# Kernel tuning notes

Measured on AMD Instinct MI355X. Metric: run time of the kernel, lower is better.

The kernel has to match this reference:

```python
import jax, jax.numpy as jnp
import numpy as np

N_NODES = 100000
N_EDGES = 1600000
IN_C, HID_C, OUT_C = 64, 64, 40


def setup_inputs() -> dict:
    key = jax.random.key(0)
    ks = jax.random.split(key, 8)
    x = jax.random.normal(ks[0], (N_NODES, IN_C), dtype=jnp.float32)
    edge_index = jax.random.randint(ks[1], (2, N_EDGES), 0, N_NODES, dtype=jnp.int32)
    s = 1.0 / np.sqrt(HID_C)
    W1 = jax.random.uniform(ks[2], (IN_C, HID_C), jnp.float32, -s, s)
    b1 = jnp.zeros((HID_C,), jnp.float32)
    Wh = jax.random.uniform(ks[3], (HID_C, HID_C), jnp.float32, -s, s)
    bh = jnp.zeros((HID_C,), jnp.float32)
    W2 = jax.random.uniform(ks[4], (HID_C, OUT_C), jnp.float32, -s, s)
    b2 = jnp.zeros((OUT_C,), jnp.float32)
    return {"x": x, "edge_index": edge_index, "W1": W1, "b1": b1,
            "Wh": Wh, "bh": bh, "W2": W2, "b2": b2}


def reference(x, edge_index, W1, b1, Wh, bh, W2, b2):
    N = x.shape[0]
    loop = jnp.arange(N, dtype=edge_index.dtype)
    # GCN normalization with self-loops: A_hat = D^-1/2 (A + I) D^-1/2
    src = jnp.concatenate([edge_index[0], loop])  # [E + N]
    dst = jnp.concatenate([edge_index[1], loop])
    deg = jax.ops.segment_sum(jnp.ones_like(dst, dtype=x.dtype), dst, num_segments=N)
    dinv = jnp.where(deg > 0, jax.lax.rsqrt(deg), 0.0)
    norm = dinv[src] * dinv[dst]  # [E + N]

    def gcn_conv(h, W, b):
        h = h @ W                              # [N, out]
        msg = h[src] * norm[:, None]           # gather + scale, [E+N, out]
        return jax.ops.segment_sum(msg, dst, num_segments=N) + b

    h = jax.nn.relu(gcn_conv(x, W1, b1))       # conv1 (dropout = identity in eval)
    h = jax.nn.relu(gcn_conv(h, Wh, bh))       # hidden_conv, layer_size=2 -> one pass
    h = gcn_conv(h, W2, b2)                    # conv2
    return jax.nn.log_softmax(h, axis=1)
```

## Files before the change

kernel.cpp:

```cpp
#include <hip/hip_runtime.h>
#include <hip/hip_bf16.h>
#include <math.h>

#define EPT 16
#define BUK 256
#define BCAP 4608
#define NBUKMAX 512
#define CAP 64

typedef _Float16 half8 __attribute__((ext_vector_type(8)));
typedef _Float16 half2v __attribute__((ext_vector_type(2)));
typedef float f32x4 __attribute__((ext_vector_type(4)));

__device__ __forceinline__ unsigned short f16r(float f) {
    _Float16 h = (_Float16)f;
    return __builtin_bit_cast(unsigned short, h);
}
__device__ __forceinline__ half2v h2(unsigned u) {
    return __builtin_bit_cast(half2v, u);
}


__launch_bounds__(256, 8)
__global__ void scat1_kernel(const int* __restrict__ src, const int* __restrict__ dst,
                             int* __restrict__ cntg, unsigned* __restrict__ ebuf,
                             int E, int nbuk) {
    __shared__ int lh[NBUKMAX];
    __shared__ int lbase[NBUKMAX];
    int tid = threadIdx.x;
    for (int k = tid; k < nbuk; k += 256) lh[k] = 0;
    __syncthreads();
    int base = blockIdx.x * (256 * EPT);
    int ds[EPT], ss[EPT];
#pragma unroll
    for (int k = 0; k < EPT; ++k) {
        int e = base + k * 256 + tid;
        ds[k] = (e < E) ? dst[e] : -1;
        ss[k] = (e < E) ? src[e] : 0;
    }
#pragma unroll
    for (int k = 0; k < EPT; ++k) {
        if (ds[k] >= 0) atomicAdd(&lh[ds[k] >> 8], 1);
    }
    __syncthreads();
    for (int k = tid; k < nbuk; k += 256) {
        int c = lh[k];
        if (c > 0) lbase[k] = atomicAdd(&cntg[k], c);
        lh[k] = 0;
    }
    __syncthreads();
#pragma unroll
    for (int k = 0; k < EPT; ++k) {
        if (ds[k] >= 0) {
            int b = ds[k] >> 8;
            int pos = lbase[b] + atomicAdd(&lh[b], 1);
            if (pos < BCAP)
                ebuf[(size_t)b * BCAP + pos] = ((unsigned)ss[k] << 8) | (unsigned)(ds[k] & 255);
        }
    }
}


__global__ void build_kernel(const unsigned* __restrict__ ebuf, const int* __restrict__ cntg,
                             int* __restrict__ deg, int* __restrict__ col, int N) {
    __shared__ int hist[BUK];
    __shared__ int cur[BUK];
    int b = blockIdx.x;
    int tid = threadIdx.x;
    int cnt = cntg[b];
    if (cnt > BCAP) cnt = BCAP;
    hist[tid] = 0;
    __syncthreads();
    size_t rbase = (size_t)b * BCAP;
    for (int j = tid; j < cnt; j += 256) {
        atomicAdd(&hist[ebuf[rbase + j] & 255u], 1);
    }
    __syncthreads();
    int node = (b << 8) + tid;
    int d = hist[tid];
    if (d > CAP) d = CAP;
    if (node < N) deg[node] = d;
    cur[tid] = node << 6;
    __syncthreads();
    for (int j = tid; j < cnt; j += 256) {
        unsigned rec = ebuf[rbase + j];
        int ln = rec & 255u;
        int pos = atomicAdd(&cur[ln], 1);
        if (pos < ((((b << 8) + ln) << 6) + CAP)) col[pos] = (int)(rec >> 8);
    }
}


__global__ void prep_kernel(const int* __restrict__ deg, float* __restrict__ dinv,
                            const float* __restrict__ x, unsigned short* __restrict__ xb,
                            const float* __restrict__ W1, const float* __restrict__ Wh,
                            const float* __restrict__ W2, unsigned short* __restrict__ wp1,
                            unsigned short* __restrict__ wph, unsigned short* __restrict__ wp2,
                            int N, int zrow) {
    int bid = blockIdx.x;
    int tid = threadIdx.x;
    if (bid < 16) {
        int i = bid * 256 + tid;
        int j = i & 7;
        int lane = (i >> 3) & 63;
        int hh = (i >> 9) & 1;
        int t = i >> 10;
        int k = hh * 32 + (lane >> 4) * 8 + j;
        int cc = t * 16 + (lane & 15);
        wp1[i] = f16r(W1[k * 64 + cc]);
        wph[i] = f16r(Wh[k * 64 + cc]);
        if (t < 3) wp2[i] = f16r(cc < 40 ? W2[k * 40 + cc] : 0.f);
        if (bid == 0 && tid < 8) {
            *(uint4*)(xb + (size_t)zrow * 64 + tid * 8) = make_uint4(0, 0, 0, 0);
        }
        return;
    }
    int i = (bid - 16) * 256 + tid;
    if (i < N * 16) {
        int node = i >> 4;
        float dn = rsqrtf((float)deg[node] + 1.0f);
        if ((i & 15) == 0) dinv[node] = dn;
        float4 vv = ((const float4*)x)[(size_t)node * 16 + (i & 15)];
        ushort4 o;
        o.x = f16r(vv.x * dn); o.y = f16r(vv.y * dn);
        o.z = f16r(vv.z * dn); o.w = f16r(vv.w * dn);
        ((ushort4*)xb)[(size_t)node * 16 + (i & 15)] = o;
    }
}


__launch_bounds__(256, 8)
__global__ void fused_relu_kernel(const unsigned short* __restrict__ h,
                                  const int* __restrict__ degA,
                                  const int* __restrict__ col,
                                  const float* __restrict__ dinv,
                                  const unsigned short* __restrict__ wp,
                                  const float* __restrict__ bias,
                                  unsigned short* __restrict__ out,
                                  int n, int zrow) {
    __shared__ unsigned short tile[16][72];
    if (blockIdx.x == 0 && threadIdx.x < 8) {
        *(uint4*)(out + (size_t)zrow * 64 + threadIdx.x * 8) = make_uint4(0, 0, 0, 0);
    }
    int tid = threadIdx.x;
    int w = tid >> 6;
    int lane = tid & 63;
    int g = lane >> 4;
    int li = lane & 15;
    int sub = li >> 3;
    unsigned choff = (li & 7) * 16u;
    int nodeBase = blockIdx.x * 16;
    int row = w * 4 + g;
    int node = nodeBase + row;

    int beg = node << 6;
    int deg = -1;
    float di = 0.f;
    if (node < n) {
        deg = degA[node];
        di = dinv[node];
    }
    int total = deg + 1;
    int nb = (total + 15) >> 4;
    nb = max(nb, __shfl_xor(nb, 16));
    nb = max(nb, __shfl_xor(nb, 32));

    half2v a0 = (half2v)0, a1 = (half2v)0, a2 = (half2v)0, a3 = (half2v)0;
    half2v c0 = (half2v)0, c1 = (half2v)0, c2 = (half2v)0, c3 = (half2v)0;

    int idx;
    {
        int e0 = li;
        idx = zrow;
        if (e0 < deg) idx = col[beg + e0];
        else if (e0 == deg) idx = node;
    }
    for (int b = 0; b < nb; ++b) {
        int nidx = zrow;
        if (b + 1 < nb) {
            int e0 = ((b + 1) << 4) + li;
            if (e0 < deg) nidx = col[beg + e0];
            else if (e0 == deg) nidx = node;
        }
        uint4 u[8];
#pragma unroll
        for (int it = 0; it < 8; ++it) {
            int s = __shfl(idx, (g << 4) + it * 2 + sub);
            u[it] = *(const uint4*)((const char*)h + (((unsigned)s << 7) + choff));
        }
        __builtin_amdgcn_sched_barrier(0);
#pragma unroll
        for (int it = 0; it < 8; ++it) {
            if (it & 1) { c0 += h2(u[it].x); c1 += h2(u[it].y); c2 += h2(u[it].z); c3 += h2(u[it].w); }
            else        { a0 += h2(u[it].x); a1 += h2(u[it].y); a2 += h2(u[it].z); a3 += h2(u[it].w); }
        }
        idx = nidx;
    }
    a0 += c0; a1 += c1; a2 += c2; a3 += c3;
    a0 += __builtin_bit_cast(half2v, __shfl_xor(__builtin_bit_cast(int, a0), 8));
    a1 += __builtin_bit_cast(half2v, __shfl_xor(__builtin_bit_cast(int, a1), 8));
    a2 += __builtin_bit_cast(half2v, __shfl_xor(__builtin_bit_cast(int, a2), 8));
    a3 += __builtin_bit_cast(half2v, __shfl_xor(__builtin_bit_cast(int, a3), 8));

    if (sub == 0) {
        half2v dih = __builtin_bit_cast(half2v, __builtin_amdgcn_cvt_pkrtz(di, di));
        a0 *= dih; a1 *= dih; a2 *= dih; a3 *= dih;
        uint4 o;
        o.x = __builtin_bit_cast(unsigned, a0);
        o.y = __builtin_bit_cast(unsigned, a1);
        o.z = __builtin_bit_cast(unsigned, a2);
        o.w = __builtin_bit_cast(unsigned, a3);
        *(uint4*)((char*)&tile[row][0] + choff) = o;
    }
    __syncthreads();

    int q = lane >> 4, c = lane & 15;
    half8 bf0 = *(const half8*)(wp + w * 1024 + lane * 8);
    half8 bf1 = *(const half8*)(wp + w * 1024 + 512 + lane * 8);
    float bs = bias[w * 16 + c];
    half8 fa0 = *(const half8*)&tile[c][q * 8];
    half8 fa1 = *(const half8*)&tile[c][32 + q * 8];
    f32x4 z = {0.f, 0.f, 0.f, 0.f};
    z = __builtin_amdgcn_mfma_f32_16x16x32_f16(fa0, bf0, z, 0, 0, 0);
    z = __builtin_amdgcn_mfma_f32_16x16x32_f16(fa1, bf1, z, 0, 0, 0);
#pragma unroll
    for (int r = 0; r < 4; ++r) {
        int nodeW = nodeBase + q * 4 + r;
        if (nodeW < n) {
            float dn = dinv[nodeW];
            out[(size_t)nodeW * 64 + w * 16 + c] = f16r(fmaxf(z[r] + bs, 0.f) * dn);
        }
    }
}


__launch_bounds__(256, 8)
__global__ void fused_lsm_kernel(const unsigned short* __restrict__ h,
                                 const int* __restrict__ degA,
                                 const int* __restrict__ col,
                                 const float* __restrict__ dinv,
                                 const unsigned short* __restrict__ wp,
                                 const float* __restrict__ bias,
                                 float* __restrict__ out,
                                 int n, int zrow) {
    __shared__ unsigned short tile[16][72];
    int tid = threadIdx.x;
    int w = tid >> 6;
    int lane = tid & 63;
    int g = lane >> 4;
    int li = lane & 15;
    int sub = li >> 3;
    unsigned choff = (li & 7) * 16u;
    int nodeBase = blockIdx.x * 16;
    int row = w * 4 + g;
    int node = nodeBase + row;

    int beg = node << 6;
    int deg = -1;
    float di = 0.f;
    if (node < n) {
        deg = degA[node];
        di = dinv[node];
    }
    int total = deg + 1;
    int nb = (total + 15) >> 4;
    nb = max(nb, __shfl_xor(nb, 16));
    nb = max(nb, __shfl_xor(nb, 32));

    half2v a0 = (half2v)0, a1 = (half2v)0, a2 = (half2v)0, a3 = (half2v)0;
    half2v c0a = (half2v)0, c1a = (half2v)0, c2a = (half2v)0, c3a = (half2v)0;

    int idx;
    {
        int e0 = li;
        idx = zrow;
        if (e0 < deg) idx = col[beg + e0];
        else if (e0 == deg) idx = node;
    }
    for (int b = 0; b < nb; ++b) {
        int nidx = zrow;
        if (b + 1 < nb) {
            int e0 = ((b + 1) << 4) + li;
            if (e0 < deg) nidx = col[beg + e0];
            else if (e0 == deg) nidx = node;
        }
        uint4 u[8];
#pragma unroll
        for (int it = 0; it < 8; ++it) {
            int s = __shfl(idx, (g << 4) + it * 2 + sub);
            u[it] = *(const uint4*)((const char*)h + (((unsigned)s << 7) + choff));
        }
        __builtin_amdgcn_sched_barrier(0);
#pragma unroll
        for (int it = 0; it < 8; ++it) {
            if (it & 1) { c0a += h2(u[it].x); c1a += h2(u[it].y); c2a += h2(u[it].z); c3a += h2(u[it].w); }
            else        { a0 += h2(u[it].x);  a1 += h2(u[it].y);  a2 += h2(u[it].z);  a3 += h2(u[it].w); }
        }
        idx = nidx;
    }
    a0 += c0a; a1 += c1a; a2 += c2a; a3 += c3a;
    a0 += __builtin_bit_cast(half2v, __shfl_xor(__builtin_bit_cast(int, a0), 8));
    a1 += __builtin_bit_cast(half2v, __shfl_xor(__builtin_bit_cast(int, a1), 8));
    a2 += __builtin_bit_cast(half2v, __shfl_xor(__builtin_bit_cast(int, a2), 8));
    a3 += __builtin_bit_cast(half2v, __shfl_xor(__builtin_bit_cast(int, a3), 8));

    if (sub == 0) {
        half2v dih = __builtin_bit_cast(half2v, __builtin_amdgcn_cvt_pkrtz(di, di));
        a0 *= dih; a1 *= dih; a2 *= dih; a3 *= dih;
        uint4 o;
        o.x = __builtin_bit_cast(unsigned, a0);
        o.y = __builtin_bit_cast(unsigned, a1);
        o.z = __builtin_bit_cast(unsigned, a2);
        o.w = __builtin_bit_cast(unsigned, a3);
        *(uint4*)((char*)&tile[row][0] + choff) = o;
    }
    __syncthreads();
    if (w != 0) return;

    int q = lane >> 4, c = lane & 15;
    bool v2ok = (c < 8);

    half8 bfrag[3][2];
#pragma unroll
    for (int t = 0; t < 3; ++t)
#pragma unroll
        for (int hh = 0; hh < 2; ++hh)
            bfrag[t][hh] = *(const half8*)(wp + t * 1024 + hh * 512 + lane * 8);
    float bs[3];
    bs[0] = bias[c];
    bs[1] = bias[16 + c];
    bs[2] = v2ok ? bias[32 + c] : 0.f;

    half8 fa0 = *(const half8*)&tile[c][q * 8];
    half8 fa1 = *(const half8*)&tile[c][32 + q * 8];

    f32x4 acc[3];
#pragma unroll
    for (int t = 0; t < 3; ++t) {
        f32x4 z = {0.f, 0.f, 0.f, 0.f};
        z = __builtin_amdgcn_mfma_f32_16x16x32_f16(fa0, bfrag[t][0], z, 0, 0, 0);
        z = __builtin_amdgcn_mfma_f32_16x16x32_f16(fa1, bfrag[t][1], z, 0, 0, 0);
        acc[t] = z;
    }

#pragma unroll
    for (int r = 0; r < 4; ++r) {
        int nodeW = nodeBase + q * 4 + r;
        if (nodeW < n) {
            float v0 = acc[0][r] + bs[0];
            float v1 = acc[1][r] + bs[1];
            float v2 = v2ok ? (acc[2][r] + bs[2]) : -INFINITY;
            float m = fmaxf(fmaxf(v0, v1), v2);
#pragma unroll
            for (int off = 1; off <= 8; off <<= 1) m = fmaxf(m, __shfl_xor(m, off));
            float s = expf(v0 - m) + expf(v1 - m) + (v2ok ? expf(v2 - m) : 0.f);
#pragma unroll
            for (int off = 1; off <= 8; off <<= 1) s += __shfl_xor(s, off);
            float ls = m + logf(s);
            float* orow = out + (size_t)nodeW * 40;
            orow[c] = v0 - ls;
            orow[16 + c] = v1 - ls;
            if (v2ok) orow[32 + c] = v2 - ls;
        }
    }
}


extern "C" void kernel_launch(void* const* d_in, const int* in_sizes, int n_in,
                              void* d_out, int out_size, void* d_ws, size_t ws_size,
                              hipStream_t stream) {
    const float* x  = (const float*)d_in[0];
    const int* ei   = (const int*)d_in[1];
    const float* W1 = (const float*)d_in[2];
    const float* b1 = (const float*)d_in[3];
    const float* Wh = (const float*)d_in[4];
    const float* bh = (const float*)d_in[5];
    const float* W2 = (const float*)d_in[6];
    const float* b2 = (const float*)d_in[7];
    float* out = (float*)d_out;

    const int N = in_sizes[0] / 64;
    const int E = in_sizes[1] / 2;
    const int nblk = (E + 256 * EPT - 1) / (256 * EPT);
    const int nbuk = (N + BUK - 1) / BUK;
    const int nTiles = (N + 15) / 16;
    const int Npad = nTiles * 16;

    const int* srcp = ei;
    const int* dstp = ei + E;

    size_t off = 0;
    auto alloc = [&](size_t bytes) {
        size_t o = off;
        off = (off + bytes + 255) & ~(size_t)255;
        return o;
    };
    char* ws = (char*)d_ws;
    int*      cntg    = (int*)(ws + alloc((size_t)nbuk * 4));
    int*      deg     = (int*)(ws + alloc((size_t)N * 4));
    float*    dinv    = (float*)(ws + alloc((size_t)N * 4));
    int*      col     = (int*)(ws + alloc((size_t)N * CAP * 4));
    unsigned* ebuf    = (unsigned*)(ws + alloc((size_t)nbuk * BCAP * 4));
    unsigned short* wp1  = (unsigned short*)(ws + alloc(4096 * 2));
    unsigned short* wph  = (unsigned short*)(ws + alloc(4096 * 2));
    unsigned short* wp2  = (unsigned short*)(ws + alloc(3072 * 2));
    unsigned short* xb   = (unsigned short*)(ws + alloc((size_t)(Npad + 1) * 64 * 2));
    unsigned short* gA   = (unsigned short*)(ws + alloc((size_t)(Npad + 1) * 64 * 2));
    unsigned short* gB   = (unsigned short*)(ws + alloc((size_t)(Npad + 1) * 64 * 2));
    (void)ws_size;

    hipMemsetAsync(cntg, 0, (size_t)nbuk * 4, stream);

    scat1_kernel<<<nblk, 256, 0, stream>>>(srcp, dstp, cntg, ebuf, E, nbuk);
    build_kernel<<<nbuk, 256, 0, stream>>>(ebuf, cntg, deg, col, N);
    prep_kernel<<<16 + (N * 16 + 255) / 256, 256, 0, stream>>>(deg, dinv, x, xb,
                                                               W1, Wh, W2, wp1, wph, wp2,
                                                               N, Npad);

    fused_relu_kernel<<<nTiles, 256, 0, stream>>>(xb, deg, col, dinv, wp1, b1, gA, N, Npad);
    fused_relu_kernel<<<nTiles, 256, 0, stream>>>(gA, deg, col, dinv, wph, bh, gB, N, Npad);
    fused_lsm_kernel<<<nTiles, 256, 0, stream>>>(gB, deg, col, dinv, wp2, b2, out, N, Npad);
}
```

Before: 226.0 us.

## Fold prep kernel into scatter and build kernels to cut launches

The separate prep kernel is removed. Weight packing and zero-row init move into extra blocks of the scatter kernel, and the dinv computation plus the x scaling and fp16 conversion move into the tail of the build kernel, using per-bucket degrees kept in shared memory. This saves one kernel launch and one global read of deg. The trade-off is that build now runs only 391 blocks that each convert 256 rows of x, which is less parallelism for that conversion than the former wide grid.

New measurement: 232.8 us. +3.0%, slower.

```diff
diff --git a/kernel.cpp b/kernel.cpp
--- a/kernel.cpp
+++ b/kernel.cpp
@@ -22,84 +22,16 @@
 
 
 __launch_bounds__(256, 8)
-__global__ void scat1_kernel(const int* __restrict__ src, const int* __restrict__ dst,
-                             int* __restrict__ cntg, unsigned* __restrict__ ebuf,
-                             int E, int nbuk) {
-    __shared__ int lh[NBUKMAX];
-    __shared__ int lbase[NBUKMAX];
+__global__ void scat1_pack_kernel(const int* __restrict__ src, const int* __restrict__ dst,
+                                  int* __restrict__ cntg, unsigned* __restrict__ ebuf,
+                                  const float* __restrict__ W1, const float* __restrict__ Wh,
+                                  const float* __restrict__ W2, unsigned short* __restrict__ wp1,
+                                  unsigned short* __restrict__ wph, unsigned short* __restrict__ wp2,
+                                  unsigned short* __restrict__ xb, int zrow,
+                                  int E, int nblk, int nbuk) {
     int tid = threadIdx.x;
-    for (int k = tid; k < nbuk; k += 256) lh[k] = 0;
-    __syncthreads();
-    int base = blockIdx.x * (256 * EPT);
-    int ds[EPT], ss[EPT];
-#pragma unroll
-    for (int k = 0; k < EPT; ++k) {
-        int e = base + k * 256 + tid;
-        ds[k] = (e < E) ? dst[e] : -1;
-        ss[k] = (e < E) ? src[e] : 0;
-    }
-#pragma unroll
-    for (int k = 0; k < EPT; ++k) {
-        if (ds[k] >= 0) atomicAdd(&lh[ds[k] >> 8], 1);
-    }
-    __syncthreads();
-    for (int k = tid; k < nbuk; k += 256) {
-        int c = lh[k];
-        if (c > 0) lbase[k] = atomicAdd(&cntg[k], c);
-        lh[k] = 0;
-    }
-    __syncthreads();
-#pragma unroll
-    for (int k = 0; k < EPT; ++k) {
-        if (ds[k] >= 0) {
-            int b = ds[k] >> 8;
-            int pos = lbase[b] + atomicAdd(&lh[b], 1);
-            if (pos < BCAP)
-                ebuf[(size_t)b * BCAP + pos] = ((unsigned)ss[k] << 8) | (unsigned)(ds[k] & 255);
-        }
-    }
-}
-
-
-__global__ void build_kernel(const unsigned* __restrict__ ebuf, const int* __restrict__ cntg,
-                             int* __restrict__ deg, int* __restrict__ col, int N) {
-    __shared__ int hist[BUK];
-    __shared__ int cur[BUK];
-    int b = blockIdx.x;
-    int tid = threadIdx.x;
-    int cnt = cntg[b];
-    if (cnt > BCAP) cnt = BCAP;
-    hist[tid] = 0;
-    __syncthreads();
-    size_t rbase = (size_t)b * BCAP;
-    for (int j = tid; j < cnt; j += 256) {
-        atomicAdd(&hist[ebuf[rbase + j] & 255u], 1);
-    }
-    __syncthreads();
-    int node = (b << 8) + tid;
-    int d = hist[tid];
-    if (d > CAP) d = CAP;
-    if (node < N) deg[node] = d;
-    cur[tid] = node << 6;
-    __syncthreads();
-    for (int j = tid; j < cnt; j += 256) {
-        unsigned rec = ebuf[rbase + j];
-        int ln = rec & 255u;
-        int pos = atomicAdd(&cur[ln], 1);
-        if (pos < ((((b << 8) + ln) << 6) + CAP)) col[pos] = (int)(rec >> 8);
-    }
-}
-
-
-__global__ void prep_kernel(const int* __restrict__ deg, float* __restrict__ dinv,
-                            const float* __restrict__ x, unsigned short* __restrict__ xb,
-                            const float* __restrict__ W1, const float* __restrict__ Wh,
-                            const float* __restrict__ W2, unsigned short* __restrict__ wp1,
-                            unsigned short* __restrict__ wph, unsigned short* __restrict__ wp2,
-                            int N, int zrow) {
-    int bid = blockIdx.x;
-    int tid = threadIdx.x;
-    if (bid < 16) {
+    if ((int)blockIdx.x >= nblk) {
+        int bid = blockIdx.x - nblk;
         int i = bid * 256 + tid;
         int j = i & 7;
         int lane = (i >> 3) & 63;
@@ -115,16 +47,86 @@
         }
         return;
     }
-    int i = (bid - 16) * 256 + tid;
-    if (i < N * 16) {
-        int node = i >> 4;
-        float dn = rsqrtf((float)deg[node] + 1.0f);
-        if ((i & 15) == 0) dinv[node] = dn;
-        float4 vv = ((const float4*)x)[(size_t)node * 16 + (i & 15)];
-        ushort4 o;
-        o.x = f16r(vv.x * dn); o.y = f16r(vv.y * dn);
-        o.z = f16r(vv.z * dn); o.w = f16r(vv.w * dn);
-        ((ushort4*)xb)[(size_t)node * 16 + (i & 15)] = o;
+
+    __shared__ int lh[NBUKMAX];
+    __shared__ int lbase[NBUKMAX];
+    for (int k = tid; k < nbuk; k += 256) lh[k] = 0;
+    __syncthreads();
+    int base = blockIdx.x * (256 * EPT);
+    int ds[EPT], ss[EPT];
+#pragma unroll
+    for (int k = 0; k < EPT; ++k) {
+        int e = base + k * 256 + tid;
+        ds[k] = (e < E) ? dst[e] : -1;
+        ss[k] = (e < E) ? src[e] : 0;
+    }
+#pragma unroll
+    for (int k = 0; k < EPT; ++k) {
+        if (ds[k] >= 0) atomicAdd(&lh[ds[k] >> 8], 1);
+    }
+    __syncthreads();
+    for (int k = tid; k < nbuk; k += 256) {
+        int c = lh[k];
+        if (c > 0) lbase[k] = atomicAdd(&cntg[k], c);
+        lh[k] = 0;
+    }
+    __syncthreads();
+#pragma unroll
+    for (int k = 0; k < EPT; ++k) {
+        if (ds[k] >= 0) {
+            int b = ds[k] >> 8;
+            int pos = lbase[b] + atomicAdd(&lh[b], 1);
+            if (pos < BCAP)
+                ebuf[(size_t)b * BCAP + pos] = ((unsigned)ss[k] << 8) | (unsigned)(ds[k] & 255);
+        }
+    }
+}
+
+
+__global__ void build_kernel(const unsigned* __restrict__ ebuf, const int* __restrict__ cntg,
+                             int* __restrict__ deg, float* __restrict__ dinv,
+                             const float* __restrict__ x, unsigned short* __restrict__ xb,
+                             int* __restrict__ col, int N) {
+    __shared__ int hist[BUK];
+    __shared__ int cur[BUK];
+    __shared__ float dl[BUK];
+    int b = blockIdx.x;
+    int tid = threadIdx.x;
+    int cnt = cntg[b];
+    if (cnt > BCAP) cnt = BCAP;
+    hist[tid] = 0;
+    __syncthreads();
+    size_t rbase = (size_t)b * BCAP;
+    for (int j = tid; j < cnt; j += 256) {
+        atomicAdd(&hist[ebuf[rbase + j] & 255u], 1);
+    }
+    __syncthreads();
+    int node = (b << 8) + tid;
+    int d = hist[tid];
+    if (d > CAP) d = CAP;
+    float df = rsqrtf((float)d + 1.0f);
+    if (node < N) { deg[node] = d; dinv[node] = df; }
+    dl[tid] = df;
+    cur[tid] = node << 6;
+    __syncthreads();
+    for (int j = tid; j < cnt; j += 256) {
+        unsigned rec = ebuf[rbase + j];
+        int ln = rec & 255u;
+        int pos = atomicAdd(&cur[ln], 1);
+        if (pos < ((((b << 8) + ln) << 6) + CAP)) col[pos] = (int)(rec >> 8);
+    }
+    int nodeBase = b << 8;
+    for (int g = tid; g < BUK * 16; g += 256) {
+        int rr = g >> 4;
+        int node2 = nodeBase + rr;
+        if (node2 < N) {
+            float dn = dl[rr];
+            float4 vv = ((const float4*)x)[(size_t)node2 * 16 + (g & 15)];
+            ushort4 o;
+            o.x = f16r(vv.x * dn); o.y = f16r(vv.y * dn);
+            o.z = f16r(vv.z * dn); o.w = f16r(vv.w * dn);
+            ((ushort4*)xb)[(size_t)node2 * 16 + (g & 15)] = o;
+        }
     }
 }
 
@@ -411,11 +413,10 @@
 
     hipMemsetAsync(cntg, 0, (size_t)nbuk * 4, stream);
 
-    scat1_kernel<<<nblk, 256, 0, stream>>>(srcp, dstp, cntg, ebuf, E, nbuk);
-    build_kernel<<<nbuk, 256, 0, stream>>>(ebuf, cntg, deg, col, N);
-    prep_kernel<<<16 + (N * 16 + 255) / 256, 256, 0, stream>>>(deg, dinv, x, xb,
-                                                               W1, Wh, W2, wp1, wph, wp2,
-                                                               N, Npad);
+    scat1_pack_kernel<<<nblk + 16, 256, 0, stream>>>(srcp, dstp, cntg, ebuf,
+                                                     W1, Wh, W2, wp1, wph, wp2,
+                                                     xb, Npad, E, nblk, nbuk);
+    build_kernel<<<nbuk, 256, 0, stream>>>(ebuf, cntg, deg, dinv, x, xb, col, N);
 
     fused_relu_kernel<<<nTiles, 256, 0, stream>>>(xb, deg, col, dinv, wp1, b1, gA, N, Npad);
     fused_relu_kernel<<<nTiles, 256, 0, stream>>>(gA, deg, col, dinv, wph, bh, gB, N, Npad);
```
